# Kernel tuning notes

Hardware: AMD Instinct MI355X
Metric: run time of the kernel (lower is better)

The kernel has to match this reference:

```python
import jax, jax.numpy as jnp
import numpy as np

B, T = 4, 2048
IN_DIM = 128          # eff_in_dim == eff_out_dim (n_groups = 1)
IN_POINTS = 32
OUT_POINTS = 32
QUERY_DIM = 256
OUT_QUERY_DIM = 256
HIDDEN = QUERY_DIM // 4                       # 64
CHANNEL_PARAMS = IN_DIM * IN_DIM              # 16384
SPATIAL_PARAMS = OUT_POINTS * IN_POINTS       # 1024
TOTAL_PARAMS = CHANNEL_PARAMS + SPATIAL_PARAMS  # 17408
LN_EPS = 1e-6


def setup_inputs() -> dict:
    key = jax.random.key(0)
    ks = jax.random.split(key, 10)
    inp = {
        "sampled": jax.random.normal(ks[0], (B, T, 1, IN_POINTS, IN_DIM), jnp.float32),
        "query": jax.random.normal(ks[1], (B, T, QUERY_DIM), jnp.float32),
        # parameter_generator: LayerNorm(QUERY_DIM) -> Linear(QUERY_DIM, HIDDEN) -> Linear(HIDDEN, TOTAL_PARAMS)
        "ln_w": jnp.ones((QUERY_DIM,), jnp.float32) * QUERY_DIM ** -0.5,
        "ln_b": jnp.zeros((QUERY_DIM,), jnp.float32),
        "w1": jax.random.normal(ks[2], (HIDDEN, QUERY_DIM), jnp.float32) * 0.05,
        "b1": jax.random.normal(ks[3], (HIDDEN,), jnp.float32) * 0.02,
        "w2": jax.random.normal(ks[4], (TOTAL_PARAMS, HIDDEN), jnp.float32) * 0.05,
        "b2": jax.random.normal(ks[5], (TOTAL_PARAMS,), jnp.float32) * 0.05,
        "m_beta": jnp.zeros((IN_DIM,), jnp.float32),
        "s_beta": jnp.zeros((OUT_POINTS,), jnp.float32),
        "wo": jax.random.normal(ks[6], (OUT_QUERY_DIM, IN_DIM * OUT_POINTS), jnp.float32) * 0.02,
        "bo": jax.random.normal(ks[7], (OUT_QUERY_DIM,), jnp.float32) * 0.02,
    }
    return inp


def reference(sampled, query, ln_w, ln_b, w1, b1, w2, b2, m_beta, s_beta, wo, bo):
    b, t, g, P, C = sampled.shape  # g == 1
    BT = b * t
    OP = s_beta.shape[0]

    # parameter generator: LN -> Linear -> Linear (no activation in between)
    mu = jnp.mean(query, axis=-1, keepdims=True)
    var = jnp.var(query, axis=-1, keepdims=True)
    q = (query - mu) * jax.lax.rsqrt(var + LN_EPS) * ln_w + ln_b
    h = q @ w1.T + b1                               # [B, T, HIDDEN]
    params = (h @ w2.T + b2).reshape(BT, -1)        # [BT, TOTAL_PARAMS]

    channel_mixing = params[:, : C * C].reshape(BT, C, C)      # [BT, C, C]
    spatial_mixing = params[:, C * C :].reshape(BT, OP, P)     # [BT, OP, P]

    x = sampled.reshape(BT, P, C)
    # channel mixing: baddbmm(m_beta, x, channel_mixing) then GELU (exact/erf)
    x = jax.nn.gelu(jnp.einsum("bpc,bcd->bpd", x, channel_mixing) + m_beta,
                    approximate=False)
    # spatial mixing: baddbmm(s_beta, spatial_mixing, x) then GELU
    x = jax.nn.gelu(jnp.einsum("bop,bpd->bod", spatial_mixing, x) + s_beta[:, None],
                    approximate=False)

    out = x.reshape(b, t, -1) @ wo.T + bo           # [B, T, OUT_QUERY_DIM]
    return out
```

## Files before the change

kernel.cpp:

```cpp
#include <hip/hip_runtime.h>
#include <hip/hip_bf16.h>
#include <cstdint>


typedef __bf16 bf16x8 __attribute__((ext_vector_type(8)));
typedef float  f32x4  __attribute__((ext_vector_type(4)));
typedef unsigned short ushort;
typedef ushort ushort8 __attribute__((ext_vector_type(8)));

#define TW 16

__device__ __forceinline__ uint32_t pk2(float a, float b) {
    __hip_bfloat162 h = __float22bfloat162_rn(make_float2(a, b));
    uint32_t r;
    __builtin_memcpy(&r, &h, 4);
    return r;
}
__device__ __forceinline__ ushort f2b(float f) {
    return (ushort)pk2(f, f);
}
__device__ __forceinline__ bf16x8 cvt8(float4 lo, float4 hi) {
    uint4 u;
    u.x = pk2(lo.x, lo.y); u.y = pk2(lo.z, lo.w);
    u.z = pk2(hi.x, hi.y); u.w = pk2(hi.z, hi.w);
    return __builtin_bit_cast(bf16x8, u);
}
__device__ __forceinline__ float gelu_fast(float x) {
    float z = fabsf(x) * 0.70710678118654752440f;
    float t = __builtin_amdgcn_rcpf(fmaf(0.3275911f, z, 1.0f));
    float p = t * fmaf(t, fmaf(t, fmaf(t, fmaf(t, 1.061405429f, -1.453152027f),
                                       1.421413741f), -0.284496736f), 0.254829592f);
    float e = __expf(-z * z);
    float erfv = copysignf(fmaf(-p, e, 1.0f), x);
    return 0.5f * x * (1.0f + erfv);
}

__device__ __forceinline__ int g2swz(int t, int d16, int byte) {
    return (t * 1024 + d16 * 64 + byte) ^ (((t ^ d16) & 7) << 4);
}

__global__ void prep(const float* __restrict__ w2, const float* __restrict__ w1,
                     const float* __restrict__ wo, const float* __restrict__ b2,
                     ushort* __restrict__ w2p, ushort* __restrict__ w2sp,
                     ushort* __restrict__ w1p, ushort* __restrict__ wop,
                     float* __restrict__ b2t) {
    const int blk = blockIdx.x, tid = threadIdx.x;
    if (blk < 512) {
        int i8 = blk * 256 + tid;
        int l = i8 & 63, ks = (i8 >> 6) & 1, d = (i8 >> 7) & 127, cb = i8 >> 14;
        int c = cb * 16 + (l & 15);
        const float* src = w2 + (size_t)(c * 128 + d) * 64 + ks * 32 + (l >> 4) * 8;
        bf16x8 u = cvt8(*(const float4*)src, *(const float4*)(src + 4));
        *(bf16x8*)&w2p[(size_t)i8 * 8] = u;
    } else if (blk < 1024) {
        int t8 = (blk - 512) * 256 + tid;
        int dcol = t8 & 127, o3 = (t8 >> 7) & 3, q = t8 >> 9;
        const float* src = wo + (size_t)q * 4096 + o3 * 1024 + dcol;
        float4 lo, hi;
        lo.x = src[0 * 128]; lo.y = src[1 * 128]; lo.z = src[2 * 128]; lo.w = src[3 * 128];
        hi.x = src[4 * 128]; hi.y = src[5 * 128]; hi.z = src[6 * 128]; hi.w = src[7 * 128];
        bf16x8 u = cvt8(lo, hi);
        *(bf16x8*)&wop[(size_t)dcol * 8192 + (q >> 4) * 512 + (q & 15) * 8 + o3 * 128] = u;
    } else if (blk < 1056) {
        int t = (blk - 1024) * 256 + tid;
        int l = t & 63, ks = (t >> 6) & 1, g = t >> 7;
        const float* src = w2 + (size_t)(16384 + g * 16 + (l & 15)) * 64 +
                           ks * 32 + (l >> 4) * 8;
        bf16x8 u = cvt8(*(const float4*)src, *(const float4*)(src + 4));
        *(bf16x8*)&w2sp[(size_t)t * 8] = u;
    } else if (blk < 1064) {
        int t = (blk - 1056) * 256 + tid;
        int l = t & 63, ks = (t >> 6) & 7, nb = t >> 9;
        const float* src = w1 + (nb * 16 + (l & 15)) * 256 + ks * 32 + (l >> 4) * 8;
        bf16x8 u = cvt8(*(const float4*)src, *(const float4*)(src + 4));
        *(bf16x8*)&w1p[(size_t)t * 8] = u;
    } else {
        int t = (blk - 1064) * 256 + tid;
        int d = t & 127, c4 = t >> 7;
        float4 r;
        r.x = b2[(c4 * 4 + 0) * 128 + d];
        r.y = b2[(c4 * 4 + 1) * 128 + d];
        r.z = b2[(c4 * 4 + 2) * 128 + d];
        r.w = b2[(c4 * 4 + 3) * 128 + d];
        *(float4*)&b2t[d * 128 + c4 * 4] = r;
    }
}

__launch_bounds__(512, 2)
__global__ void fused(const float* __restrict__ sampled, const float* __restrict__ query,
                      const float* __restrict__ ln_w, const float* __restrict__ ln_b,
                      const float* __restrict__ b1, const float* __restrict__ b2,
                      const float* __restrict__ m_beta, const float* __restrict__ s_beta,
                      const ushort* __restrict__ w2p, const ushort* __restrict__ w2sp,
                      const ushort* __restrict__ w1p, const float* __restrict__ b2t,
                      const ushort* __restrict__ wop, const float* __restrict__ bo,
                      float* __restrict__ out) {
    __shared__ union {
        ushort qn[TW * 264];
        ushort smT[TW * 1032];
        struct {
            ushort pt[TW * 1032];
            ushort g1s[TW * 640];
        } mp;
    } U;
    __shared__ __align__(16) union {
        ushort Hb[TW * 64];
        ushort g2t[TW * 16 * 32];
    } G;
    __shared__ float mb_s[128];
    __shared__ float sb_s[32];

    const int tid  = threadIdx.x;
    const int wv   = tid >> 6;
    const int lane = tid & 63;
    const int lq   = lane >> 4;
    const int ln16 = lane & 15;
    const int tok0 = blockIdx.x * TW;

    if (tid < 128) mb_s[tid] = m_beta[tid];
    else if (tid < 160) sb_s[tid - 128] = s_beta[tid - 128];

    for (int tt = 0; tt < 2; ++tt) {
        int t = wv * 2 + tt;
        const float* q = query + (size_t)(tok0 + t) * 256;
        float2 a = *(const float2*)(q + 2 * lane);
        float2 b = *(const float2*)(q + 128 + 2 * lane);
        float s = a.x + a.y + b.x + b.y;
        for (int off = 1; off < 64; off <<= 1) s += __shfl_xor(s, off);
        float mu = s * (1.0f / 256.0f);
        float d0 = a.x - mu, d1 = a.y - mu, d2 = b.x - mu, d3 = b.y - mu;
        float ss = d0 * d0 + d1 * d1 + d2 * d2 + d3 * d3;
        for (int off = 1; off < 64; off <<= 1) ss += __shfl_xor(ss, off);
        float rstd = rsqrtf(ss * (1.0f / 256.0f) + 1e-6f);
        int i0 = 2 * lane, i1 = 2 * lane + 128;
        float q0 = d0 * rstd * ln_w[i0]     + ln_b[i0];
        float q1 = d1 * rstd * ln_w[i0 + 1] + ln_b[i0 + 1];
        float q2 = d2 * rstd * ln_w[i1]     + ln_b[i1];
        float q3 = d3 * rstd * ln_w[i1 + 1] + ln_b[i1 + 1];
        *(uint32_t*)&U.qn[t * 264 + i0] = pk2(q0, q1);
        *(uint32_t*)&U.qn[t * 264 + i1] = pk2(q2, q3);
    }
    __syncthreads();

    if (wv < 4) {
        int nb = wv;
        f32x4 acc = {0.0f, 0.0f, 0.0f, 0.0f};
        for (int ks = 0; ks < 8; ++ks) {
            bf16x8 afr = *(const bf16x8*)&U.qn[ln16 * 264 + ks * 32 + lq * 8];
            bf16x8 bfr = *(const bf16x8*)&w1p[(nb * 8 + ks) * 512 + lane * 8];
            acc = __builtin_amdgcn_mfma_f32_16x16x32_bf16(afr, bfr, acc, 0, 0, 0);
        }
        float bias = b1[nb * 16 + ln16];
        for (int i = 0; i < 4; ++i) {
            int t = lq * 4 + i;
            G.Hb[t * 64 + nb * 16 + ln16] = f2b(acc[i] + bias);
        }
    }
    __syncthreads();

    bf16x8 hfr[2];
    hfr[0] = *(const bf16x8*)&G.Hb[ln16 * 64 + 0 + lq * 8];
    hfr[1] = *(const bf16x8*)&G.Hb[ln16 * 64 + 32 + lq * 8];

    for (int gi = 0; gi < 8; ++gi) {
        int g = wv * 8 + gi;
        f32x4 acc = *(const f32x4*)&b2[16384 + g * 16 + lq * 4];
        for (int ks = 0; ks < 2; ++ks) {
            bf16x8 afr = *(const bf16x8*)&w2sp[(g * 2 + ks) * 512 + lane * 8];
            acc = __builtin_amdgcn_mfma_f32_16x16x32_bf16(afr, hfr[ks], acc, 0, 0, 0);
        }
        int o = g >> 1;
        int p0 = (g & 1) * 16 + lq * 4;
        uint2 wr;
        wr.x = pk2(acc[0], acc[1]);
        wr.y = pk2(acc[2], acc[3]);
        *(uint2*)&U.smT[ln16 * 1032 + o * 32 + p0] = wr;
    }

    bf16x8 xa[2][2][4];
    for (int tt = 0; tt < 2; ++tt) {
        const float* xp = sampled + (size_t)(tok0 + wv * 2 + tt) * 4096;
        for (int mt = 0; mt < 2; ++mt) {
            int p = mt * 16 + ln16;
            for (int ks = 0; ks < 4; ++ks) {
                int c = ks * 32 + lq * 8;
                xa[tt][mt][ks] = cvt8(*(const float4*)(xp + p * 128 + c),
                                      *(const float4*)(xp + p * 128 + c + 4));
            }
        }
    }
    __syncthreads();

    bf16x8 sa[2][2];
    for (int tt = 0; tt < 2; ++tt) {
        int t = wv * 2 + tt;
        for (int mt = 0; mt < 2; ++mt)
            sa[tt][mt] = *(const bf16x8*)&U.smT[t * 1032 + (mt * 16 + ln16) * 32 + lq * 8];
    }
    __syncthreads();

    f32x4 aco[2] = {(f32x4){0.0f, 0.0f, 0.0f, 0.0f}, (f32x4){0.0f, 0.0f, 0.0f, 0.0f}};

    auto outacc = [&](int dt2) {
        const ushort* wb = wop + ((size_t)(dt2 * 16) * 16 + wv * 2) * 512 + lane * 8;
        bf16x8 nb0 = *(const bf16x8*)(wb);
        bf16x8 nb1 = *(const bf16x8*)(wb + 512);
        for (int d16 = 0; d16 < 16; ++d16) {
            bf16x8 b0 = nb0, b1 = nb1;
            if (d16 < 15) {
                nb0 = *(const bf16x8*)(wb + (size_t)(d16 + 1) * 8192);
                nb1 = *(const bf16x8*)(wb + (size_t)(d16 + 1) * 8192 + 512);
            }
            bf16x8 afr = *(const bf16x8*)((const char*)G.g2t + g2swz(ln16, d16, lq * 16));
            aco[0] = __builtin_amdgcn_mfma_f32_16x16x32_bf16(afr, b0, aco[0], 0, 0, 0);
            aco[1] = __builtin_amdgcn_mfma_f32_16x16x32_bf16(afr, b1, aco[1], 0, 0, 0);
        }
    };

    for (int dt = 0; dt < 16; ++dt) {
        if (dt && !(dt & 1)) outacc((dt >> 1) - 1);

        const int cb = wv;
        for (int dd = 0; dd < 8; ++dd) {
            int d = dt * 8 + dd;
            f32x4 acc = *(const f32x4*)&b2t[d * 128 + cb * 16 + lq * 4];
            for (int ks = 0; ks < 2; ++ks) {
                bf16x8 afr = *(const bf16x8*)&w2p[((cb * 128 + d) * 2 + ks) * 512 + lane * 8];
                acc = __builtin_amdgcn_mfma_f32_16x16x32_bf16(afr, hfr[ks], acc, 0, 0, 0);
            }
            uint2 wr;
            wr.x = pk2(acc[0], acc[1]);
            wr.y = pk2(acc[2], acc[3]);
            *(uint2*)&U.mp.pt[ln16 * 1032 + ((cb * 2 + (lq >> 1)) * 8 + dd) * 8 + (lq & 1) * 4] = wr;
        }
        __syncthreads();

        const int ddl = ln16 & 7;
        const bool hi = ln16 >= 8;
        for (int tt = 0; tt < 2; ++tt) {
            int t = wv * 2 + tt;
            bf16x8 bfr[4];
            for (int ks = 0; ks < 4; ++ks)
                bfr[ks] = *(const bf16x8*)&U.mp.pt[t * 1032 + (ks * 4 + lq) * 64 + ddl * 8];
            float mb = mb_s[dt * 8 + ddl];
            for (int mt = 0; mt < 2; ++mt) {
                f32x4 acc = {0.0f, 0.0f, 0.0f, 0.0f};
                for (int ks = 0; ks < 4; ++ks)
                    acc = __builtin_amdgcn_mfma_f32_16x16x32_bf16(xa[tt][mt][ks], bfr[ks], acc, 0, 0, 0);
                float va = hi ? acc[2] : acc[0];
                float vb = hi ? acc[3] : acc[1];
                float ga = gelu_fast(va + mb);
                float gb = gelu_fast(vb + mb);
                int p = mt * 16 + lq * 4 + (hi ? 2 : 0);
                *(uint32_t*)&U.mp.g1s[t * 640 + ((dt & 1) * 8 + ddl) * 40 + p] = pk2(ga, gb);
            }
        }

        if (dt & 1) {
            __builtin_amdgcn_wave_barrier();
            for (int tt = 0; tt < 2; ++tt) {
                int t = wv * 2 + tt;
                bf16x8 gfr = *(const bf16x8*)&U.mp.g1s[t * 640 + ln16 * 40 + lq * 8];
                for (int mt = 0; mt < 2; ++mt) {
                    f32x4 acc = {0.0f, 0.0f, 0.0f, 0.0f};
                    acc = __builtin_amdgcn_mfma_f32_16x16x32_bf16(sa[tt][mt], gfr, acc, 0, 0, 0);
                    float4 sbv = *(const float4*)&sb_s[mt * 16 + lq * 4];
                    float g0 = gelu_fast(acc[0] + sbv.x);
                    float g1 = gelu_fast(acc[1] + sbv.y);
                    float g2 = gelu_fast(acc[2] + sbv.z);
                    float g3 = gelu_fast(acc[3] + sbv.w);
                    uint2 wr;
                    wr.x = pk2(g0, g1);
                    wr.y = pk2(g2, g3);
                    *(uint2*)((char*)G.g2t + g2swz(t, ln16, mt * 32 + lq * 8)) = wr;
                }
            }
        }
        __syncthreads();
    }

    outacc(7);
    for (int n = 0; n < 2; ++n) {
        int q = (wv * 2 + n) * 16 + ln16;
        float bv = bo[q];
        for (int i = 0; i < 4; ++i) {
            int tok = tok0 + lq * 4 + i;
            out[(size_t)tok * 256 + q] = aco[n][i] + bv;
        }
    }
}

extern "C" void kernel_launch(void* const* d_in, const int* in_sizes, int n_in,
                              void* d_out, int out_size, void* d_ws, size_t ws_size,
                              hipStream_t stream) {
    const float* sampled = (const float*)d_in[0];
    const float* query   = (const float*)d_in[1];
    const float* ln_w    = (const float*)d_in[2];
    const float* ln_b    = (const float*)d_in[3];
    const float* w1      = (const float*)d_in[4];
    const float* b1      = (const float*)d_in[5];
    const float* w2      = (const float*)d_in[6];
    const float* b2      = (const float*)d_in[7];
    const float* m_beta  = (const float*)d_in[8];
    const float* s_beta  = (const float*)d_in[9];
    const float* wo      = (const float*)d_in[10];
    const float* bo      = (const float*)d_in[11];
    float* out = (float*)d_out;

    char* ws = (char*)d_ws;
    ushort* w2p  = (ushort*)(ws);
    ushort* wop  = (ushort*)(ws + 2097152);
    ushort* w2sp = (ushort*)(ws + 4194304);
    ushort* w1p  = (ushort*)(ws + 4325376);
    float*  b2t  = (float*) (ws + 4358144);

    prep<<<1080, 256, 0, stream>>>(w2, w1, wo, b2, w2p, w2sp, w1p, wop, b2t);
    fused<<<512, 512, 0, stream>>>(sampled, query, ln_w, ln_b, b1, b2,
                                   m_beta, s_beta, w2p, w2sp, w1p, b2t,
                                   wop, bo, out);
}
```

Before: 378.7 us.

## Pre-convert sampled activations to bf16 in prep kernel and reload per channel tile

Moves the fp32-to-bf16 conversion of the sampled tensor into the prep kernel, writing it in MFMA fragment order to workspace. The fused kernel no longer keeps 16 bf16x8 x-fragments live in registers across the whole channel loop. Instead it reloads them from global memory in every channel tile. This aims to cut register pressure and improve occupancy. In exchange it adds a full extra read and write pass over the activations, plus repeated global reloads inside the loop.

```diff
diff --git a/kernel.cpp b/kernel.cpp
--- a/kernel.cpp
+++ b/kernel.cpp
@@ -39,21 +39,32 @@
     return (t * 1024 + d16 * 64 + byte) ^ (((t ^ d16) & 7) << 4);
 }
 
-__global__ void prep(const float* __restrict__ w2, const float* __restrict__ w1,
+__global__ void prep(const float* __restrict__ sampled,
+                     const float* __restrict__ w2, const float* __restrict__ w1,
                      const float* __restrict__ wo, const float* __restrict__ b2,
                      ushort* __restrict__ w2p, ushort* __restrict__ w2sp,
                      ushort* __restrict__ w1p, ushort* __restrict__ wop,
-                     float* __restrict__ b2t) {
+                     float* __restrict__ b2t, ushort* __restrict__ xp) {
     const int blk = blockIdx.x, tid = threadIdx.x;
-    if (blk < 512) {
+    if (blk < 16384) {
         int i8 = blk * 256 + tid;
+        int l = i8 & 63, ks = (i8 >> 6) & 3, mt = (i8 >> 8) & 1, t = i8 >> 9;
+        int p = mt * 16 + (l & 15), c0 = ks * 32 + (l >> 4) * 8;
+        const float* src = sampled + (size_t)t * 4096 + p * 128 + c0;
+        bf16x8 u = cvt8(*(const float4*)src, *(const float4*)(src + 4));
+        *(bf16x8*)&xp[(size_t)i8 * 8] = u;
+        return;
+    }
+    const int blkr = blk - 16384;
+    if (blkr < 512) {
+        int i8 = blkr * 256 + tid;
         int l = i8 & 63, ks = (i8 >> 6) & 1, d = (i8 >> 7) & 127, cb = i8 >> 14;
         int c = cb * 16 + (l & 15);
         const float* src = w2 + (size_t)(c * 128 + d) * 64 + ks * 32 + (l >> 4) * 8;
         bf16x8 u = cvt8(*(const float4*)src, *(const float4*)(src + 4));
         *(bf16x8*)&w2p[(size_t)i8 * 8] = u;
-    } else if (blk < 1024) {
-        int t8 = (blk - 512) * 256 + tid;
+    } else if (blkr < 1024) {
+        int t8 = (blkr - 512) * 256 + tid;
         int dcol = t8 & 127, o3 = (t8 >> 7) & 3, q = t8 >> 9;
         const float* src = wo + (size_t)q * 4096 + o3 * 1024 + dcol;
         float4 lo, hi;
@@ -61,21 +72,21 @@
         hi.x = src[4 * 128]; hi.y = src[5 * 128]; hi.z = src[6 * 128]; hi.w = src[7 * 128];
         bf16x8 u = cvt8(lo, hi);
         *(bf16x8*)&wop[(size_t)dcol * 8192 + (q >> 4) * 512 + (q & 15) * 8 + o3 * 128] = u;
-    } else if (blk < 1056) {
-        int t = (blk - 1024) * 256 + tid;
+    } else if (blkr < 1056) {
+        int t = (blkr - 1024) * 256 + tid;
         int l = t & 63, ks = (t >> 6) & 1, g = t >> 7;
         const float* src = w2 + (size_t)(16384 + g * 16 + (l & 15)) * 64 +
                            ks * 32 + (l >> 4) * 8;
         bf16x8 u = cvt8(*(const float4*)src, *(const float4*)(src + 4));
         *(bf16x8*)&w2sp[(size_t)t * 8] = u;
-    } else if (blk < 1064) {
-        int t = (blk - 1056) * 256 + tid;
+    } else if (blkr < 1064) {
+        int t = (blkr - 1056) * 256 + tid;
         int l = t & 63, ks = (t >> 6) & 7, nb = t >> 9;
         const float* src = w1 + (nb * 16 + (l & 15)) * 256 + ks * 32 + (l >> 4) * 8;
         bf16x8 u = cvt8(*(const float4*)src, *(const float4*)(src + 4));
         *(bf16x8*)&w1p[(size_t)t * 8] = u;
     } else {
-        int t = (blk - 1064) * 256 + tid;
+        int t = (blkr - 1064) * 256 + tid;
         int d = t & 127, c4 = t >> 7;
         float4 r;
         r.x = b2[(c4 * 4 + 0) * 128 + d];
@@ -87,7 +98,7 @@
 }
 
 __launch_bounds__(512, 2)
-__global__ void fused(const float* __restrict__ sampled, const float* __restrict__ query,
+__global__ void fused(const ushort* __restrict__ xp, const float* __restrict__ query,
                       const float* __restrict__ ln_w, const float* __restrict__ ln_b,
                       const float* __restrict__ b1, const float* __restrict__ b2,
                       const float* __restrict__ m_beta, const float* __restrict__ s_beta,
@@ -176,19 +187,6 @@
         wr.y = pk2(acc[2], acc[3]);
         *(uint2*)&U.smT[ln16 * 1032 + o * 32 + p0] = wr;
     }
-
-    bf16x8 xa[2][2][4];
-    for (int tt = 0; tt < 2; ++tt) {
-        const float* xp = sampled + (size_t)(tok0 + wv * 2 + tt) * 4096;
-        for (int mt = 0; mt < 2; ++mt) {
-            int p = mt * 16 + ln16;
-            for (int ks = 0; ks < 4; ++ks) {
-                int c = ks * 32 + lq * 8;
-                xa[tt][mt][ks] = cvt8(*(const float4*)(xp + p * 128 + c),
-                                      *(const float4*)(xp + p * 128 + c + 4));
-            }
-        }
-    }
     __syncthreads();
 
     bf16x8 sa[2][2];
@@ -239,6 +237,11 @@
         const bool hi = ln16 >= 8;
         for (int tt = 0; tt < 2; ++tt) {
             int t = wv * 2 + tt;
+            const ushort* xpt = xp + (size_t)(tok0 + t) * 4096 + lane * 8;
+            bf16x8 xf[2][4];
+            for (int mt = 0; mt < 2; ++mt)
+                for (int ks = 0; ks < 4; ++ks)
+                    xf[mt][ks] = *(const bf16x8*)(xpt + (mt * 4 + ks) * 512);
             bf16x8 bfr[4];
             for (int ks = 0; ks < 4; ++ks)
                 bfr[ks] = *(const bf16x8*)&U.mp.pt[t * 1032 + (ks * 4 + lq) * 64 + ddl * 8];
@@ -246,7 +249,7 @@
             for (int mt = 0; mt < 2; ++mt) {
                 f32x4 acc = {0.0f, 0.0f, 0.0f, 0.0f};
                 for (int ks = 0; ks < 4; ++ks)
-                    acc = __builtin_amdgcn_mfma_f32_16x16x32_bf16(xa[tt][mt][ks], bfr[ks], acc, 0, 0, 0);
+                    acc = __builtin_amdgcn_mfma_f32_16x16x32_bf16(xf[mt][ks], bfr[ks], acc, 0, 0, 0);
                 float va = hi ? acc[2] : acc[0];
                 float vb = hi ? acc[3] : acc[1];
                 float ga = gelu_fast(va + mb);
@@ -313,9 +316,11 @@
     ushort* w2sp = (ushort*)(ws + 4194304);
     ushort* w1p  = (ushort*)(ws + 4325376);
     float*  b2t  = (float*) (ws + 4358144);
-
-    prep<<<1080, 256, 0, stream>>>(w2, w1, wo, b2, w2p, w2sp, w1p, wop, b2t);
-    fused<<<512, 512, 0, stream>>>(sampled, query, ln_w, ln_b, b1, b2,
+    ushort* xp   = (ushort*)(ws + 4423680);
+
+    prep<<<17464, 256, 0, stream>>>(sampled, w2, w1, wo, b2,
+                                    w2p, w2sp, w1p, wop, b2t, xp);
+    fused<<<512, 512, 0, stream>>>(xp, query, ln_w, ln_b, b1, b2,
                                    m_beta, s_beta, w2p, w2sp, w1p, b2t,
                                    wop, bo, out);
 }
```

Result: slower. 395.8 us (+4.5%).
